# Kernel tuning notes

Hardware: AMD Instinct MI355X
Metric: run time of the kernel (lower is better)

Reference implementation:

```python
import jax, jax.numpy as jnp
import numpy as np

N_HEADS = 16


def _rope_tables(seq_len, head_dim, dtype):
    # matches torch RoPE.__init__: inv_freq over head_dim, outer with positions
    inv_freq = 1.0 / (10000.0 ** (jnp.arange(0, head_dim, 2, dtype=jnp.float32) / head_dim))
    t = jnp.arange(seq_len, dtype=jnp.float32)
    freqs = jnp.outer(t, inv_freq)  # [T, head_dim//2]
    return jnp.cos(freqs).astype(dtype), jnp.sin(freqs).astype(dtype)


def _apply_rope(x, cos, sin):
    # x: [B, H, T, Dh]; interleaved even/odd rotation
    x_even = x[..., ::2]
    x_odd = x[..., 1::2]
    rot_even = x_even * cos - x_odd * sin
    rot_odd = x_even * sin + x_odd * cos
    return jnp.stack([rot_even, rot_odd], axis=-1).reshape(x.shape)


def setup_inputs() -> dict:
    key = jax.random.key(0)
    ks = jax.random.split(key, 5)
    B, T, D = 4, 1024, 1024
    s = 1.0 / np.sqrt(D)
    return {
        "x": jax.random.normal(ks[0], (B, T, D), dtype=jnp.float32),
        "Wq": jax.random.normal(ks[1], (D, D), dtype=jnp.float32) * s,
        "Wk": jax.random.normal(ks[2], (D, D), dtype=jnp.float32) * s,
        "Wv": jax.random.normal(ks[3], (D, D), dtype=jnp.float32) * s,
        "Wo": jax.random.normal(ks[4], (D, D), dtype=jnp.float32) * s,
    }


def reference(x, Wq, Wk, Wv, Wo):
    B, T, D = x.shape
    H = N_HEADS
    Dh = D // H

    def proj(W):
        # nn.Linear: x @ W.T ; reshape to [B, H, T, Dh]
        return (x @ W.T).reshape(B, T, H, Dh).transpose(0, 2, 1, 3)

    q, k, v = proj(Wq), proj(Wk), proj(Wv)
    cos, sin = _rope_tables(T, Dh, x.dtype)
    q = _apply_rope(q, cos, sin)
    k = _apply_rope(k, cos, sin)

    # NOTE: original module applies NO 1/sqrt(Dh) scaling
    scores = jnp.einsum("bhqd,bhkd->bhqk", q, k)
    causal = jnp.tril(jnp.ones((T, T), dtype=bool))
    scores = jnp.where(causal, scores, -jnp.inf)
    attn = jax.nn.softmax(scores, axis=-1)
    out = jnp.einsum("bhqk,bhkd->bhqd", attn, v)
    out = out.transpose(0, 2, 1, 3).reshape(B, T, D)
    return out @ Wo.T
```

## Files before the change

kernel.cpp:

```cpp
#include <hip/hip_runtime.h>
#include <stdint.h>

typedef unsigned short u16;
typedef short s16x8 __attribute__((ext_vector_type(8)));
typedef __bf16 bf16x8 __attribute__((ext_vector_type(8)));
typedef _Float16 f16x8 __attribute__((ext_vector_type(8)));
typedef float f32x4 __attribute__((ext_vector_type(4)));

#define SEQ    1024
#define DMODEL 1024
#define NB     4
#define NH     16
#define DH     64
#define QBLK   128
#define KVB    64
#define LOG2E  1.4426950408889634f

__device__ __forceinline__ u16 f2bf(float f) {
  uint32_t u = __builtin_bit_cast(uint32_t, f);
  u += 0x7fffu + ((u >> 16) & 1u);
  return (u16)(u >> 16);
}
__device__ __forceinline__ u16 f2bf_rz(float f) {
  return (u16)(__builtin_bit_cast(uint32_t, f) >> 16);
}
__device__ __forceinline__ float bf2f(u16 h) {
  uint32_t u = ((uint32_t)h) << 16;
  return __builtin_bit_cast(float, u);
}
__device__ __forceinline__ u16 f2h(float f) {
  return __builtin_bit_cast(u16, (_Float16)f);
}
__device__ __forceinline__ float h2f(u16 u) {
  return (float)__builtin_bit_cast(_Float16, u);
}

#define MFMA16(a, b, c)  __builtin_amdgcn_mfma_f32_16x16x32_bf16((a), (b), (c), 0, 0, 0)
#define MFMA16H(a, b, c) __builtin_amdgcn_mfma_f32_16x16x32_f16((a), (b), (c), 0, 0, 0)

template<bool F16>
__device__ __forceinline__ f32x4 MF(s16x8 a, s16x8 b, f32x4 c) {
  if constexpr (F16)
    return MFMA16H(__builtin_bit_cast(f16x8, a), __builtin_bit_cast(f16x8, b), c);
  else
    return MFMA16(__builtin_bit_cast(bf16x8, a), __builtin_bit_cast(bf16x8, b), c);
}

__device__ __forceinline__ void gload_lds16(const u16* g, uintptr_t lds_addr) {
  __builtin_amdgcn_global_load_lds(
      (__attribute__((address_space(1))) void*)(uintptr_t)g,
      (__attribute__((address_space(3))) void*)lds_addr,
      16, 0, 0);
}

__global__ void cast_bf_kernel(const float* __restrict__ src, u16* __restrict__ dst, int n8) {
  int i = blockIdx.x * blockDim.x + threadIdx.x;
  if (i >= n8) return;
  float4 v0 = *(const float4*)(src + (size_t)i * 8);
  float4 v1 = *(const float4*)(src + (size_t)i * 8 + 4);
  union { u16 u[8]; uint4 v; } H;
  H.u[0] = f2bf(v0.x); H.u[1] = f2bf(v0.y); H.u[2] = f2bf(v0.z); H.u[3] = f2bf(v0.w);
  H.u[4] = f2bf(v1.x); H.u[5] = f2bf(v1.y); H.u[6] = f2bf(v1.z); H.u[7] = f2bf(v1.w);
  *(uint4*)(dst + (size_t)i * 8) = H.v;
}

__global__ void cast_h_kernel(const float* __restrict__ src, u16* __restrict__ dst, int n8) {
  int i = blockIdx.x * blockDim.x + threadIdx.x;
  if (i >= n8) return;
  float4 v0 = *(const float4*)(src + (size_t)i * 8);
  float4 v1 = *(const float4*)(src + (size_t)i * 8 + 4);
  union { u16 u[8]; uint4 v; } H;
  H.u[0] = f2h(v0.x); H.u[1] = f2h(v0.y); H.u[2] = f2h(v0.z); H.u[3] = f2h(v0.w);
  H.u[4] = f2h(v1.x); H.u[5] = f2h(v1.y); H.u[6] = f2h(v1.z); H.u[7] = f2h(v1.w);
  *(uint4*)(dst + (size_t)i * 8) = H.v;
}

__global__ void rope_kernel(u16* __restrict__ Q, u16* __restrict__ K) {
  const int nP = (NB * SEQ) * (DMODEL / 2);
  int idx = blockIdx.x * blockDim.x + threadIdx.x;
  u16* buf; int p;
  if (idx < nP) { buf = Q; p = idx; }
  else          { buf = K; p = idx - nP; }
  int row = p >> 9;
  int pi  = p & 511;
  int t   = row & (SEQ - 1);
  int fi  = pi & 31;
  float inv = exp2f((float)fi * (-13.287712379549449f / 32.0f));
  float ang = (float)t * inv;
  float sn, cs;
  sincosf(ang, &sn, &cs);
  size_t off = (size_t)row * DMODEL + pi * 2;
  uint32_t v = *(uint32_t*)(buf + off);
  float e = h2f((u16)(v & 0xffffu));
  float o = h2f((u16)(v >> 16));
  float re = e * cs - o * sn;
  float ro = e * sn + o * cs;
  *(uint32_t*)(buf + off) = (uint32_t)f2h(re) | ((uint32_t)f2h(ro) << 16);
}

__global__ void add_kernel(const float* __restrict__ p0, const float* __restrict__ p1,
                           float* __restrict__ out, int n8) {
  int i = blockIdx.x * blockDim.x + threadIdx.x;
  if (i >= n8) return;
  float4 a0 = *(const float4*)(p0 + (size_t)i * 8);
  float4 a1 = *(const float4*)(p0 + (size_t)i * 8 + 4);
  float4 b0 = *(const float4*)(p1 + (size_t)i * 8);
  float4 b1 = *(const float4*)(p1 + (size_t)i * 8 + 4);
  float4 c0 = make_float4(a0.x + b0.x, a0.y + b0.y, a0.z + b0.z, a0.w + b0.w);
  float4 c1 = make_float4(a1.x + b1.x, a1.y + b1.y, a1.z + b1.z, a1.w + b1.w);
  *(float4*)(out + (size_t)i * 8) = c0;
  *(float4*)(out + (size_t)i * 8 + 4) = c1;
}

struct GemmPtrs {
  const u16* B[3]; u16* C0[3]; int mode[3];
};

template<bool F16>
__global__ __launch_bounds__(256) void gemm_bt_kernel(
    const u16* __restrict__ A,
    GemmPtrs P, float* __restrict__ CF,
    int M, int N, int K, int out_f32)
{
  __shared__ __align__(16) u16 sA[128 * 64];
  __shared__ __align__(16) u16 sB[128 * 64];
  const int t = threadIdx.x, lane = t & 63;
  const int wave = t >> 6;
  const int g = lane >> 4, cl = lane & 15;
  const int z = blockIdx.z;
  const u16* B = P.B[z];
  const int n0 = blockIdx.x * 128, m0 = blockIdx.y * 128;
  const int wr = wave >> 1, wc = wave & 1;

  int kb = 0, ke = K;
  if (out_f32) {
    int kc = K / gridDim.z;
    kb = z * kc; ke = kb + kc;
    CF += (size_t)z * M * N;
  }

  int srow[4], scol[4], soff[4];
#pragma unroll
  for (int j = 0; j < 4; ++j) {
    int c = j * 256 + t;
    srow[j] = c >> 3;
    scol[j] = ((c & 7) ^ (srow[j] & 7)) * 8;
    soff[j] = c * 16;
  }

  f32x4 acc[4][4] = {};

  for (int k0 = kb; k0 < ke; k0 += 64) {
#pragma unroll
    for (int j = 0; j < 4; ++j) {
      gload_lds16(A + (size_t)(m0 + srow[j]) * K + k0 + scol[j], (uintptr_t)sA + soff[j]);
      gload_lds16(B + (size_t)(n0 + srow[j]) * K + k0 + scol[j], (uintptr_t)sB + soff[j]);
    }
    __syncthreads();

    s16x8 af[4][2];
#pragma unroll
    for (int m = 0; m < 4; ++m) {
      int row = wr * 64 + m * 16 + cl;
#pragma unroll
      for (int kk = 0; kk < 2; ++kk)
        af[m][kk] = *(const s16x8*)&sA[row * 64 + (((kk * 4 + g) ^ (row & 7)) * 8)];
    }
#pragma unroll
    for (int n = 0; n < 4; ++n) {
      int row = wc * 64 + n * 16 + cl;
      s16x8 b0 = *(const s16x8*)&sB[row * 64 + ((g ^ (row & 7)) * 8)];
      s16x8 b1 = *(const s16x8*)&sB[row * 64 + (((4 + g) ^ (row & 7)) * 8)];
#pragma unroll
      for (int m = 0; m < 4; ++m) {
        acc[m][n] = MF<F16>(af[m][0], b0, acc[m][n]);
        acc[m][n] = MF<F16>(af[m][1], b1, acc[m][n]);
      }
    }
    __syncthreads();
  }

  if (out_f32) {
#pragma unroll
    for (int m = 0; m < 4; ++m)
#pragma unroll
      for (int n = 0; n < 4; ++n)
#pragma unroll
        for (int r = 0; r < 4; ++r) {
          int row = m0 + wr * 64 + m * 16 + g * 4 + r;
          int col = n0 + wc * 64 + n * 16 + cl;
          CF[(size_t)row * N + col] = acc[m][n][r];
        }
  } else if (P.mode[z] == 1) {
    u16* VT = P.C0[z];
#pragma unroll
    for (int m = 0; m < 4; ++m)
#pragma unroll
      for (int n = 0; n < 4; ++n) {
        int row0 = m0 + wr * 64 + m * 16 + g * 4;
        int col = n0 + wc * 64 + n * 16 + cl;
        union { u16 u[4]; uint2 v; } pk;
#pragma unroll
        for (int r = 0; r < 4; ++r) pk.u[r] = f2bf(acc[m][n][r]);
        *(uint2*)&VT[(size_t)col * M + row0] = pk.v;
      }
  } else {
    u16* C = P.C0[z];
#pragma unroll
    for (int m = 0; m < 4; ++m)
#pragma unroll
      for (int n = 0; n < 4; ++n)
#pragma unroll
        for (int r = 0; r < 4; ++r) {
          int row = m0 + wr * 64 + m * 16 + g * 4 + r;
          int col = n0 + wc * 64 + n * 16 + cl;
          float v = acc[m][n][r];
          C[(size_t)row * N + col] = F16 ? f2h(v) : f2bf(v);
        }
  }
}

__global__ __launch_bounds__(256, 2) void attn_kernel(
    const u16* __restrict__ Q, const u16* __restrict__ K,
    const u16* __restrict__ Vt,
    u16* __restrict__ Oh)
{
  __shared__ __align__(16) u16 sK [2][KVB * 64];
  __shared__ __align__(16) u16 sVt[2][DH * KVB];
  __shared__ __align__(16) u16 sP[128 * 72];

  const int t = threadIdx.x, lane = t & 63, wave = t >> 6;
  const int g = lane >> 4, cl = lane & 15;
  const int h = blockIdx.x & (NH - 1), b = blockIdx.x >> 4;
  const int y = blockIdx.y;
  const int qi = (y < 4) ? (7 - y) : (y - 4);
  const int q0 = qi * QBLK;
  const size_t rowbase = (size_t)b * SEQ;
  const int colbase = h * DH;
  const int MT = NB * SEQ;

  const u16* Kb  = K + rowbase * DMODEL + colbase;
  const u16* Vtb = Vt + (size_t)(h * DH) * MT + b * SEQ;

  int srow[2], scol[2], soff[2];
#pragma unroll
  for (int j = 0; j < 2; ++j) {
    int c = j * 256 + t;
    srow[j] = c >> 3;
    scol[j] = ((c & 7) ^ (srow[j] & 7)) * 8;
    soff[j] = c * 16;
  }

  int koff0[4], koff1[4];
#pragma unroll
  for (int n = 0; n < 4; ++n) {
    int row = n * 16 + cl;
    koff0[n] = row * 64 + ((g ^ (row & 7)) * 8);
    koff1[n] = row * 64 + (((4 + g) ^ (row & 7)) * 8);
  }
  int paoff[2][2];
#pragma unroll
  for (int kk = 0; kk < 2; ++kk) {
    paoff[kk][0] = (wave * 32 + cl) * 72 + kk * 32 + g * 8;
    paoff[kk][1] = (wave * 32 + 16 + cl) * 72 + kk * 32 + g * 8;
  }

  f16x8 qf[2][2];
#pragma unroll
  for (int mf = 0; mf < 2; ++mf) {
    int qrow = q0 + wave * 32 + mf * 16 + cl;
    const u16* pq = Q + (rowbase + qrow) * DMODEL + colbase + g * 8;
    qf[mf][0] = __builtin_bit_cast(f16x8, *(const s16x8*)pq);
    qf[mf][1] = __builtin_bit_cast(f16x8, *(const s16x8*)(pq + 32));
  }

  bf16x8 ones;
#pragma unroll
  for (int e = 0; e < 8; ++e) ones[e] = (__bf16)1.0f;

  f32x4 o_acc[2][4] = {};
  f32x4 o_l[2] = {};

  const int last = 2 * qi + 1;
  const int wrow0 = q0 + wave * 32;
  const int prow0 = wave * 32;

#pragma unroll
  for (int j = 0; j < 2; ++j) {
    gload_lds16(Kb + (size_t)srow[j] * DMODEL + scol[j],  (uintptr_t)&sK[0][0] + soff[j]);
    gload_lds16(Vtb + (size_t)srow[j] * MT + scol[j],     (uintptr_t)&sVt[0][0] + soff[j]);
  }
  __syncthreads();

  int cur = 0;
  for (int kt = 0; kt <= last; ++kt) {
    const int kv0 = kt * KVB;
    if (kt < last) {
      const int nk = kv0 + KVB;
#pragma unroll
      for (int j = 0; j < 2; ++j) {
        gload_lds16(Kb + (size_t)(nk + srow[j]) * DMODEL + scol[j],
                    (uintptr_t)&sK[cur ^ 1][0] + soff[j]);
        gload_lds16(Vtb + (size_t)srow[j] * MT + nk + scol[j],
                    (uintptr_t)&sVt[cur ^ 1][0] + soff[j]);
      }
    }

    const bool skip = (wrow0 + 31) < kv0;
    if (!skip) {
      const bool needmask = (kv0 + 63) > wrow0;

      f32x4 s[2][4];
      __builtin_amdgcn_s_setprio(1);
#pragma unroll
      for (int n = 0; n < 4; ++n) {
        f16x8 k0 = __builtin_bit_cast(f16x8, *(const s16x8*)&sK[cur][koff0[n]]);
        f16x8 k1 = __builtin_bit_cast(f16x8, *(const s16x8*)&sK[cur][koff1[n]]);
#pragma unroll
        for (int mf = 0; mf < 2; ++mf) {
          f32x4 zz = {};
          zz = MFMA16H(qf[mf][0], k0, zz);
          zz = MFMA16H(qf[mf][1], k1, zz);
          s[mf][n] = zz;
        }
      }
      __builtin_amdgcn_s_setprio(0);

#pragma unroll
      for (int mf = 0; mf < 2; ++mf) {
#pragma unroll
        for (int r = 0; r < 4; ++r) {
          int qg = wrow0 + mf * 16 + g * 4 + r;
          int prow = prow0 + mf * 16 + g * 4 + r;
#pragma unroll
          for (int n = 0; n < 4; ++n) {
            float p = exp2f(s[mf][n][r] * LOG2E);
            if (needmask && (kv0 + n * 16 + cl > qg)) p = 0.0f;
            sP[prow * 72 + n * 16 + cl] = f2bf_rz(p);
          }
        }
      }

      __builtin_amdgcn_s_setprio(1);
#pragma unroll
      for (int kk = 0; kk < 2; ++kk) {
        bf16x8 pa0 = *(const bf16x8*)&sP[paoff[kk][0]];
        bf16x8 pa1 = *(const bf16x8*)&sP[paoff[kk][1]];
#pragma unroll
        for (int n = 0; n < 4; ++n) {
          bf16x8 vf = *(const bf16x8*)&sVt[cur][(kk == 0) ? koff0[n] : koff1[n]];
          o_acc[0][n] = MFMA16(pa0, vf, o_acc[0][n]);
          o_acc[1][n] = MFMA16(pa1, vf, o_acc[1][n]);
        }
        o_l[0] = MFMA16(pa0, ones, o_l[0]);
        o_l[1] = MFMA16(pa1, ones, o_l[1]);
      }
      __builtin_amdgcn_s_setprio(0);
    }

    __syncthreads();
    cur ^= 1;
  }

#pragma unroll
  for (int mf = 0; mf < 2; ++mf)
#pragma unroll
    for (int n = 0; n < 4; ++n)
#pragma unroll
      for (int r = 0; r < 4; ++r) {
        float ov = o_acc[mf][n][r] / o_l[mf][r];
        int qrow = q0 + wave * 32 + mf * 16 + g * 4 + r;
        size_t idx = (rowbase + qrow) * DMODEL + colbase + n * 16 + cl;
        Oh[idx] = f2bf(ov);
      }
}

extern "C" void kernel_launch(void* const* d_in, const int* in_sizes, int n_in,
                              void* d_out, int out_size, void* d_ws, size_t ws_size,
                              hipStream_t stream) {
  const float* x  = (const float*)d_in[0];
  const float* Wq = (const float*)d_in[1];
  const float* Wk = (const float*)d_in[2];
  const float* Wv = (const float*)d_in[3];
  const float* Wo = (const float*)d_in[4];
  float* out = (float*)d_out;

  const int M = NB * SEQ;
  const int D = DMODEL;
  char* ws = (char*)d_ws;
  const size_t MB = 1u << 20;
  u16* xh16 = (u16*)(ws + 0 * MB);
  u16* qh16 = (u16*)(ws + 8 * MB);
  u16* kh16 = (u16*)(ws + 16 * MB);
  u16* vt   = (u16*)(ws + 24 * MB);
  u16* oh   = (u16*)(ws + 40 * MB);
  u16* wq16 = (u16*)(ws + 48 * MB);
  u16* wk16 = (u16*)(ws + 50 * MB);
  u16* wv16 = (u16*)(ws + 52 * MB);
  u16* wob  = (u16*)(ws + 54 * MB);
  float* wo_part = (float*)(ws + 8 * MB);

  cast_h_kernel<<<(M * D / 8 + 255) / 256, 256, 0, stream>>>(x, xh16, M * D / 8);
  cast_h_kernel<<<(D * D / 8 + 255) / 256, 256, 0, stream>>>(Wq, wq16, D * D / 8);
  cast_h_kernel<<<(D * D / 8 + 255) / 256, 256, 0, stream>>>(Wk, wk16, D * D / 8);
  cast_h_kernel<<<(D * D / 8 + 255) / 256, 256, 0, stream>>>(Wv, wv16, D * D / 8);
  cast_bf_kernel<<<(D * D / 8 + 255) / 256, 256, 0, stream>>>(Wo, wob, D * D / 8);

  {
    GemmPtrs P;
    P.B[0] = wq16; P.B[1] = wk16; P.B[2] = wv16;
    P.C0[0] = qh16; P.C0[1] = kh16; P.C0[2] = vt;
    P.mode[0] = 0; P.mode[1] = 0; P.mode[2] = 1;
    gemm_bt_kernel<true><<<dim3(D / 128, M / 128, 3), 256, 0, stream>>>(
        xh16, P, nullptr, M, D, D, 0);
  }

  rope_kernel<<<(2 * M * (D / 2) + 255) / 256, 256, 0, stream>>>(qh16, kh16);

  attn_kernel<<<dim3(NH * NB, 8), 256, 0, stream>>>(qh16, kh16, vt, oh);

  {
    GemmPtrs P;
    P.B[0] = wob; P.B[1] = wob; P.B[2] = wob;
    P.C0[0] = nullptr; P.C0[1] = nullptr; P.C0[2] = nullptr;
    P.mode[0] = 0; P.mode[1] = 0; P.mode[2] = 0;
    gemm_bt_kernel<false><<<dim3(D / 128, M / 128, 2), 256, 0, stream>>>(
        oh, P, wo_part, M, D, D, 1);
    add_kernel<<<(M * D / 8 + 255) / 256, 256, 0, stream>>>(
        wo_part, wo_part + (size_t)M * D, out, M * D / 8);
  }
}
```

Baseline: 121.6 us.

## Merge cast kernels and replace split-K output GEMM with narrower N tiles

Folds the five separate fp32-to-half/bf16 cast launches into one kernel that dispatches on the flat index. The output projection no longer uses split-K across two slices with an fp32 partial buffer and a separate add kernel. Instead it uses a 128x64 tile GEMM that writes directly to the output, keeping a similar block count without the partial-sum traffic. This removes launch overhead and two full fp32 M×D round trips, at the cost of less B reuse per block in the output GEMM.

Measured after the change: 104.7 us. -13.9%, faster.

```diff
diff --git a/kernel.cpp b/kernel.cpp
--- a/kernel.cpp
+++ b/kernel.cpp
@@ -53,26 +53,32 @@
       16, 0, 0);
 }
 
-__global__ void cast_bf_kernel(const float* __restrict__ src, u16* __restrict__ dst, int n8) {
-  int i = blockIdx.x * blockDim.x + threadIdx.x;
-  if (i >= n8) return;
-  float4 v0 = *(const float4*)(src + (size_t)i * 8);
-  float4 v1 = *(const float4*)(src + (size_t)i * 8 + 4);
+__global__ void cast_all_kernel(
+    const float* __restrict__ x, const float* __restrict__ wq,
+    const float* __restrict__ wk, const float* __restrict__ wv,
+    const float* __restrict__ wo,
+    u16* __restrict__ xd, u16* __restrict__ wqd, u16* __restrict__ wkd,
+    u16* __restrict__ wvd, u16* __restrict__ wod)
+{
+  const int NX = (NB * SEQ * DMODEL) / 8;
+  const int NW = (DMODEL * DMODEL) / 8;
+  int c = blockIdx.x * blockDim.x + threadIdx.x;
+  const float* src; u16* dst; bool tobf = false;
+  if (c < NX)                { src = x;  dst = xd; }
+  else if ((c -= NX) < NW)   { src = wq; dst = wqd; }
+  else if ((c -= NW) < NW)   { src = wk; dst = wkd; }
+  else if ((c -= NW) < NW)   { src = wv; dst = wvd; }
+  else if ((c -= NW) < NW)   { src = wo; dst = wod; tobf = true; }
+  else return;
+  float f[8];
+  float4 v0 = *(const float4*)(src + (size_t)c * 8);
+  float4 v1 = *(const float4*)(src + (size_t)c * 8 + 4);
+  f[0] = v0.x; f[1] = v0.y; f[2] = v0.z; f[3] = v0.w;
+  f[4] = v1.x; f[5] = v1.y; f[6] = v1.z; f[7] = v1.w;
   union { u16 u[8]; uint4 v; } H;
-  H.u[0] = f2bf(v0.x); H.u[1] = f2bf(v0.y); H.u[2] = f2bf(v0.z); H.u[3] = f2bf(v0.w);
-  H.u[4] = f2bf(v1.x); H.u[5] = f2bf(v1.y); H.u[6] = f2bf(v1.z); H.u[7] = f2bf(v1.w);
-  *(uint4*)(dst + (size_t)i * 8) = H.v;
-}
-
-__global__ void cast_h_kernel(const float* __restrict__ src, u16* __restrict__ dst, int n8) {
-  int i = blockIdx.x * blockDim.x + threadIdx.x;
-  if (i >= n8) return;
-  float4 v0 = *(const float4*)(src + (size_t)i * 8);
-  float4 v1 = *(const float4*)(src + (size_t)i * 8 + 4);
-  union { u16 u[8]; uint4 v; } H;
-  H.u[0] = f2h(v0.x); H.u[1] = f2h(v0.y); H.u[2] = f2h(v0.z); H.u[3] = f2h(v0.w);
-  H.u[4] = f2h(v1.x); H.u[5] = f2h(v1.y); H.u[6] = f2h(v1.z); H.u[7] = f2h(v1.w);
-  *(uint4*)(dst + (size_t)i * 8) = H.v;
+#pragma unroll
+  for (int e = 0; e < 8; ++e) H.u[e] = tobf ? f2bf(f[e]) : f2h(f[e]);
+  *(uint4*)(dst + (size_t)c * 8) = H.v;
 }
 
 __global__ void rope_kernel(u16* __restrict__ Q, u16* __restrict__ K) {
@@ -98,46 +104,27 @@
   *(uint32_t*)(buf + off) = (uint32_t)f2h(re) | ((uint32_t)f2h(ro) << 16);
 }
 
-__global__ void add_kernel(const float* __restrict__ p0, const float* __restrict__ p1,
-                           float* __restrict__ out, int n8) {
-  int i = blockIdx.x * blockDim.x + threadIdx.x;
-  if (i >= n8) return;
-  float4 a0 = *(const float4*)(p0 + (size_t)i * 8);
-  float4 a1 = *(const float4*)(p0 + (size_t)i * 8 + 4);
-  float4 b0 = *(const float4*)(p1 + (size_t)i * 8);
-  float4 b1 = *(const float4*)(p1 + (size_t)i * 8 + 4);
-  float4 c0 = make_float4(a0.x + b0.x, a0.y + b0.y, a0.z + b0.z, a0.w + b0.w);
-  float4 c1 = make_float4(a1.x + b1.x, a1.y + b1.y, a1.z + b1.z, a1.w + b1.w);
-  *(float4*)(out + (size_t)i * 8) = c0;
-  *(float4*)(out + (size_t)i * 8 + 4) = c1;
-}
-
 struct GemmPtrs {
   const u16* B[3]; u16* C0[3]; int mode[3];
 };
 
-template<bool F16>
+template<bool F16, int BN>
 __global__ __launch_bounds__(256) void gemm_bt_kernel(
     const u16* __restrict__ A,
     GemmPtrs P, float* __restrict__ CF,
     int M, int N, int K, int out_f32)
 {
+  constexpr int NF = BN / 32;
+  constexpr int BCH = BN / 32;
   __shared__ __align__(16) u16 sA[128 * 64];
-  __shared__ __align__(16) u16 sB[128 * 64];
+  __shared__ __align__(16) u16 sB[BN * 64];
   const int t = threadIdx.x, lane = t & 63;
   const int wave = t >> 6;
   const int g = lane >> 4, cl = lane & 15;
   const int z = blockIdx.z;
   const u16* B = P.B[z];
-  const int n0 = blockIdx.x * 128, m0 = blockIdx.y * 128;
+  const int n0 = blockIdx.x * BN, m0 = blockIdx.y * 128;
   const int wr = wave >> 1, wc = wave & 1;
-
-  int kb = 0, ke = K;
-  if (out_f32) {
-    int kc = K / gridDim.z;
-    kb = z * kc; ke = kb + kc;
-    CF += (size_t)z * M * N;
-  }
 
   int srow[4], scol[4], soff[4];
 #pragma unroll
@@ -148,14 +135,15 @@
     soff[j] = c * 16;
   }
 
-  f32x4 acc[4][4] = {};
-
-  for (int k0 = kb; k0 < ke; k0 += 64) {
-#pragma unroll
-    for (int j = 0; j < 4; ++j) {
+  f32x4 acc[4][NF] = {};
+
+  for (int k0 = 0; k0 < K; k0 += 64) {
+#pragma unroll
+    for (int j = 0; j < 4; ++j)
       gload_lds16(A + (size_t)(m0 + srow[j]) * K + k0 + scol[j], (uintptr_t)sA + soff[j]);
+#pragma unroll
+    for (int j = 0; j < BCH; ++j)
       gload_lds16(B + (size_t)(n0 + srow[j]) * K + k0 + scol[j], (uintptr_t)sB + soff[j]);
-    }
     __syncthreads();
 
     s16x8 af[4][2];
@@ -167,8 +155,8 @@
         af[m][kk] = *(const s16x8*)&sA[row * 64 + (((kk * 4 + g) ^ (row & 7)) * 8)];
     }
 #pragma unroll
-    for (int n = 0; n < 4; ++n) {
-      int row = wc * 64 + n * 16 + cl;
+    for (int n = 0; n < NF; ++n) {
+      int row = wc * (BN / 2) + n * 16 + cl;
       s16x8 b0 = *(const s16x8*)&sB[row * 64 + ((g ^ (row & 7)) * 8)];
       s16x8 b1 = *(const s16x8*)&sB[row * 64 + (((4 + g) ^ (row & 7)) * 8)];
 #pragma unroll
@@ -184,11 +172,11 @@
 #pragma unroll
     for (int m = 0; m < 4; ++m)
 #pragma unroll
-      for (int n = 0; n < 4; ++n)
+      for (int n = 0; n < NF; ++n)
 #pragma unroll
         for (int r = 0; r < 4; ++r) {
           int row = m0 + wr * 64 + m * 16 + g * 4 + r;
-          int col = n0 + wc * 64 + n * 16 + cl;
+          int col = n0 + wc * (BN / 2) + n * 16 + cl;
           CF[(size_t)row * N + col] = acc[m][n][r];
         }
   } else if (P.mode[z] == 1) {
@@ -196,9 +184,9 @@
 #pragma unroll
     for (int m = 0; m < 4; ++m)
 #pragma unroll
-      for (int n = 0; n < 4; ++n) {
+      for (int n = 0; n < NF; ++n) {
         int row0 = m0 + wr * 64 + m * 16 + g * 4;
-        int col = n0 + wc * 64 + n * 16 + cl;
+        int col = n0 + wc * (BN / 2) + n * 16 + cl;
         union { u16 u[4]; uint2 v; } pk;
 #pragma unroll
         for (int r = 0; r < 4; ++r) pk.u[r] = f2bf(acc[m][n][r]);
@@ -209,11 +197,11 @@
 #pragma unroll
     for (int m = 0; m < 4; ++m)
 #pragma unroll
-      for (int n = 0; n < 4; ++n)
+      for (int n = 0; n < NF; ++n)
 #pragma unroll
         for (int r = 0; r < 4; ++r) {
           int row = m0 + wr * 64 + m * 16 + g * 4 + r;
-          int col = n0 + wc * 64 + n * 16 + cl;
+          int col = n0 + wc * (BN / 2) + n * 16 + cl;
           float v = acc[m][n][r];
           C[(size_t)row * N + col] = F16 ? f2h(v) : f2bf(v);
         }
@@ -398,20 +386,19 @@
   u16* wk16 = (u16*)(ws + 50 * MB);
   u16* wv16 = (u16*)(ws + 52 * MB);
   u16* wob  = (u16*)(ws + 54 * MB);
-  float* wo_part = (float*)(ws + 8 * MB);
-
-  cast_h_kernel<<<(M * D / 8 + 255) / 256, 256, 0, stream>>>(x, xh16, M * D / 8);
-  cast_h_kernel<<<(D * D / 8 + 255) / 256, 256, 0, stream>>>(Wq, wq16, D * D / 8);
-  cast_h_kernel<<<(D * D / 8 + 255) / 256, 256, 0, stream>>>(Wk, wk16, D * D / 8);
-  cast_h_kernel<<<(D * D / 8 + 255) / 256, 256, 0, stream>>>(Wv, wv16, D * D / 8);
-  cast_bf_kernel<<<(D * D / 8 + 255) / 256, 256, 0, stream>>>(Wo, wob, D * D / 8);
+
+  {
+    int total = M * D / 8 + 4 * (D * D / 8);
+    cast_all_kernel<<<(total + 255) / 256, 256, 0, stream>>>(
+        x, Wq, Wk, Wv, Wo, xh16, wq16, wk16, wv16, wob);
+  }
 
   {
     GemmPtrs P;
     P.B[0] = wq16; P.B[1] = wk16; P.B[2] = wv16;
     P.C0[0] = qh16; P.C0[1] = kh16; P.C0[2] = vt;
     P.mode[0] = 0; P.mode[1] = 0; P.mode[2] = 1;
-    gemm_bt_kernel<true><<<dim3(D / 128, M / 128, 3), 256, 0, stream>>>(
+    gemm_bt_kernel<true, 128><<<dim3(D / 128, M / 128, 3), 256, 0, stream>>>(
         xh16, P, nullptr, M, D, D, 0);
   }
 
@@ -424,9 +411,7 @@
     P.B[0] = wob; P.B[1] = wob; P.B[2] = wob;
     P.C0[0] = nullptr; P.C0[1] = nullptr; P.C0[2] = nullptr;
     P.mode[0] = 0; P.mode[1] = 0; P.mode[2] = 0;
-    gemm_bt_kernel<false><<<dim3(D / 128, M / 128, 2), 256, 0, stream>>>(
-        oh, P, wo_part, M, D, D, 1);
-    add_kernel<<<(M * D / 8 + 255) / 256, 256, 0, stream>>>(
-        wo_part, wo_part + (size_t)M * D, out, M * D / 8);
-  }
-}
+    gemm_bt_kernel<false, 64><<<dim3(D / 64, M / 128, 1), 256, 0, stream>>>(
+        oh, P, out, M, D, D, 1);
+  }
+}
```
